# Kernel tuning notes

Hardware: AMD Instinct MI355X
Metric: run time of the kernel (lower is better)

Reference implementation:

```python
import jax, jax.numpy as jnp
import numpy as np

B, S, E, H = 4, 2048, 1024, 16
D = E // H  # head_dim = 64


def setup_inputs() -> dict:
    key = jax.random.key(0)
    ks = jax.random.split(key, 5)
    return {
        "hidden_states": jax.random.normal(ks[0], (B, S, E), dtype=jnp.float32),
        "c_attn_w": jax.random.normal(ks[1], (E, 3 * E), dtype=jnp.float32) * 0.02,
        "c_attn_b": jax.random.normal(ks[2], (3 * E,), dtype=jnp.float32) * 0.02,
        "c_proj_w": jax.random.normal(ks[3], (E, E), dtype=jnp.float32) * 0.02,
        "c_proj_b": jax.random.normal(ks[4], (E,), dtype=jnp.float32) * 0.02,
    }


def reference(hidden_states, c_attn_w, c_attn_b, c_proj_w, c_proj_b):
    b, s, e = hidden_states.shape
    # Conv1D c_attn: y = x @ W + b  -> qkv [b, s, 3E]
    qkv = hidden_states @ c_attn_w + c_attn_b
    q, k, v = jnp.split(qkv, 3, axis=-1)
    # split heads -> [b, H, s, D]
    def split_heads(t):
        return t.reshape(b, s, H, D).transpose(0, 2, 1, 3)
    q, k, v = split_heads(q), split_heads(k), split_heads(v)
    # QK^T scaled by sqrt(head_dim)
    scores = jnp.einsum("bhqd,bhkd->bhqk", q, k) / jnp.sqrt(
        jnp.asarray(D, dtype=q.dtype)
    )
    # causal mask (tril), masked positions get dtype min
    causal = jnp.tril(jnp.ones((s, s), dtype=bool))[None, None]
    mask_value = jnp.finfo(scores.dtype).min
    scores = jnp.where(causal, scores, mask_value)
    attn = jax.nn.softmax(scores, axis=-1)
    # attend to values, merge heads
    out = jnp.einsum("bhqk,bhkd->bhqd", attn, v)
    out = out.transpose(0, 2, 1, 3).reshape(b, s, e)
    # Conv1D c_proj
    return out @ c_proj_w + c_proj_b
```

## Files before the change

### kernel.cpp

```cpp
#include <hip/hip_runtime.h>
#include <hip/hip_bf16.h>
#include <cstdint>
#include <cstddef>

#define BB 4
#define SS 2048
#define EE 1024
#define HH 16
#define DD 64

typedef __attribute__((ext_vector_type(8))) short bf16x8;
typedef __attribute__((ext_vector_type(4))) float f32x4;

__device__ __forceinline__ short f2bf(float f) {
    union { float f; uint32_t u; } x; x.f = f;
    uint32_t r = (x.u + 0x7fffu + ((x.u >> 16) & 1u)) >> 16;
    return (short)r;
}
__device__ __forceinline__ short f2bf_fast(float f) {
    union { float f; uint32_t u; } x; x.f = f;
    return (short)((x.u + 0x8000u) >> 16);
}

__device__ __forceinline__ void gload16(const void* g, void* l) {
    __builtin_amdgcn_global_load_lds(
        (__attribute__((address_space(1))) uint32_t*)(uintptr_t)g,
        (__attribute__((address_space(3))) uint32_t*)(uint32_t)(uintptr_t)l,
        16, 0, 0);
}

#define WAIT_BARRIER(N)                                          \
    asm volatile("s_waitcnt vmcnt(" #N ")" ::: "memory");        \
    __builtin_amdgcn_s_barrier();                                \
    __builtin_amdgcn_sched_barrier(0);

template<int CTRL>
__device__ __forceinline__ float dppmove(float v) {
    return __int_as_float(__builtin_amdgcn_update_dpp(
        0, __float_as_int(v), CTRL, 0xf, 0xf, true));
}
#define ROW_REDUCE(vals, OP)                                             \
    _Pragma("unroll") for (int _r = 0; _r < 4; ++_r) {                   \
        vals[_r] = OP(vals[_r], dppmove<0xB1>(vals[_r]));                \
        vals[_r] = OP(vals[_r], dppmove<0x4E>(vals[_r]));                \
        vals[_r] = OP(vals[_r], dppmove<0x124>(vals[_r]));               \
        vals[_r] = OP(vals[_r], dppmove<0x128>(vals[_r]));               \
    }
__device__ __forceinline__ float opmax(float a, float b) { return fmaxf(a, b); }
__device__ __forceinline__ float opsum(float a, float b) { return a + b; }

__global__ void prep_kernel(const float* __restrict__ hs, short* __restrict__ Xb,
                            const float* __restrict__ attn_w, short* __restrict__ WqkvT,
                            const float* __restrict__ proj_w, short* __restrict__ WprojT)
{
    __shared__ float ts[32][33];
    int bid = blockIdx.x;
    const int t = threadIdx.x;
    if (bid < 2048) {
        const int n4 = (BB * SS * EE) / 4;
        const int stride = 2048 * 256;
        for (int i = bid * 256 + t; i < n4; i += stride) {
            float4 v = reinterpret_cast<const float4*>(hs)[i];
            short4 o;
            o.x = f2bf(v.x); o.y = f2bf(v.y); o.z = f2bf(v.z); o.w = f2bf(v.w);
            reinterpret_cast<short4*>(Xb)[i] = o;
        }
        return;
    }
    bid -= 2048;
    const float* in; short* out; int ncols, bx, by;
    if (bid < 3072) { in = attn_w; out = WqkvT; ncols = 3 * EE; bx = bid % 96; by = bid / 96; }
    else { bid -= 3072; in = proj_w; out = WprojT; ncols = EE; bx = bid % 32; by = bid / 32; }
    const int r = t >> 3, c4 = (t & 7) * 4;
    const int n0 = bx * 32, k0 = by * 32;
    float4 v = *reinterpret_cast<const float4*>(&in[(size_t)(k0 + r) * ncols + n0 + c4]);
    ts[c4 + 0][r] = v.x; ts[c4 + 1][r] = v.y; ts[c4 + 2][r] = v.z; ts[c4 + 3][r] = v.w;
    __syncthreads();
    short4 ov;
    ov.x = f2bf(ts[r][c4 + 0]); ov.y = f2bf(ts[r][c4 + 1]);
    ov.z = f2bf(ts[r][c4 + 2]); ov.w = f2bf(ts[r][c4 + 3]);
    *reinterpret_cast<short4*>(&out[(size_t)(n0 + r) * EE + k0 + c4]) = ov;
}

template<int MODE>
__global__ __launch_bounds__(256, 2)
void gemm128(const short* __restrict__ A, const short* __restrict__ Bt,
             const float* __restrict__ bias,
             short* __restrict__ Qo, short* __restrict__ Ko, short* __restrict__ Vo,
             float* __restrict__ Co)
{
    __shared__ short As[3][4096];
    __shared__ short Bs[3][4096];
    const int tid  = threadIdx.x;
    const int lane = tid & 63, wid = tid >> 6;
    const int wr = wid >> 1, wc = wid & 1;
    const int l15 = lane & 15, lhi = lane >> 4;
    const int m0 = blockIdx.y * 128, n0 = blockIdx.x * 128;
    const int sr   = lane >> 2;
    const int scol = 8 * ((lane & 3) ^ ((lane >> 3) & 3));
    const int rdx  = (lhi ^ ((l15 >> 1) & 3)) << 4;

    f32x4 acc[4][4] = {};

#define G_STAGE(tt, bufi)                                                        \
    {                                                                            \
        const int kk = (tt) * 32;                                                \
        _Pragma("unroll")                                                        \
        for (int p = 0; p < 2; ++p) {                                            \
            const int c = wid * 2 + p;                                           \
            gload16(&A [(size_t)(m0 + c * 16 + sr) * EE + kk + scol],            \
                    (char*)&As[bufi][0] + c * 1024);                             \
            gload16(&Bt[(size_t)(n0 + c * 16 + sr) * EE + kk + scol],            \
                    (char*)&Bs[bufi][0] + c * 1024);                             \
        }                                                                        \
    }

    G_STAGE(0, 0)
    G_STAGE(1, 1)
    WAIT_BARRIER(4)

    for (int kt = 0; kt < 32; ++kt) {
        const int cur = kt % 3;
        if (kt + 2 < 32) { const int nb = (kt + 2) % 3; G_STAGE(kt + 2, nb) }

        bf16x8 af[4], bfr[4];
        #pragma unroll
        for (int mm = 0; mm < 4; ++mm)
            af[mm] = *reinterpret_cast<const bf16x8*>(
                (const char*)&As[cur][0] + (wr * 64 + mm * 16 + l15) * 64 + rdx);
        #pragma unroll
        for (int nn = 0; nn < 4; ++nn)
            bfr[nn] = *reinterpret_cast<const bf16x8*>(
                (const char*)&Bs[cur][0] + (wc * 64 + nn * 16 + l15) * 64 + rdx);
        #pragma unroll
        for (int mm = 0; mm < 4; ++mm)
            #pragma unroll
            for (int nn = 0; nn < 4; ++nn)
                acc[mm][nn] = __builtin_amdgcn_mfma_f32_16x16x32_bf16(af[mm], bfr[nn], acc[mm][nn], 0, 0, 0);

        if (kt < 30)       { WAIT_BARRIER(4) }
        else if (kt == 30) { WAIT_BARRIER(0) }
    }
#undef G_STAGE

    if (MODE == 0) {
        const int part = n0 >> 10;
        #pragma unroll
        for (int mm = 0; mm < 4; ++mm) {
            #pragma unroll
            for (int nn = 0; nn < 4; ++nn) {
                const int gcol = n0 + wc * 64 + nn * 16 + l15;
                const float bv = bias[gcol];
                const int e = gcol & 1023;
                const int h = e >> 6, d = e & 63;
                const int grow0 = m0 + wr * 64 + mm * 16 + lhi * 4;
                const int bidx = grow0 >> 11;
                const int s0 = grow0 & 2047;
                const int bh = bidx * HH + h;
                if (part == 2) {
                    short4 pk;
                    pk.x = f2bf(acc[mm][nn][0] + bv);
                    pk.y = f2bf(acc[mm][nn][1] + bv);
                    pk.z = f2bf(acc[mm][nn][2] + bv);
                    pk.w = f2bf(acc[mm][nn][3] + bv);
                    *reinterpret_cast<short4*>(&Vo[((size_t)bh * DD + d) * SS + s0]) = pk;
                } else if (part == 0) {
                    #pragma unroll
                    for (int r = 0; r < 4; ++r)
                        Qo[((size_t)bh * SS + s0 + r) * DD + d] = f2bf((acc[mm][nn][r] + bv) * 0.18033688f);
                } else {
                    #pragma unroll
                    for (int r = 0; r < 4; ++r)
                        Ko[((size_t)bh * SS + s0 + r) * DD + d] = f2bf(acc[mm][nn][r] + bv);
                }
            }
        }
    } else {
        #pragma unroll
        for (int mm = 0; mm < 4; ++mm) {
            #pragma unroll
            for (int nn = 0; nn < 4; ++nn) {
                const int gcol = n0 + wc * 64 + nn * 16 + l15;
                const float bv = bias[gcol];
                #pragma unroll
                for (int r = 0; r < 4; ++r) {
                    const int grow = m0 + wr * 64 + mm * 16 + lhi * 4 + r;
                    Co[(size_t)grow * EE + gcol] = acc[mm][nn][r] + bv;
                }
            }
        }
    }
}

__global__ __launch_bounds__(512, 2)
void attn_kernel(const short* __restrict__ Q, const short* __restrict__ K,
                 const short* __restrict__ Vt, short* __restrict__ CTX)
{
    __shared__ short Ks[2][4096];
    __shared__ short Vs[2][4096];
    __shared__ short Ps[8][1024];
    const int tid  = threadIdx.x;
    const int lane = tid & 63, wid = tid >> 6;
    const int l15 = lane & 15, lhi = lane >> 4;
    const int bid  = blockIdx.x;
    const int bh   = (bid & 7) * 8 + ((bid >> 3) & 7);
    const int pair = bid >> 6;
    const int b = bh >> 4, h = bh & 15;
    const size_t base = (size_t)bh * (SS * DD);
    const short* VtBase = Vt + (size_t)bh * (DD * SS);
    char* const pw = (char*)&Ps[wid][0];

    const int srow = lane >> 3;
    const int scol = 8 * ((lane & 7) ^ srow);

    for (int phase = 0; phase < 2; ++phase) {
        const int t = phase ? (15 - pair) : pair;
        const int q0 = t * 128;
        const int qbase = q0 + wid * 16;
        const int nkt = 2 * t + 2;

        bf16x8 qa[2];
        qa[0] = *reinterpret_cast<const bf16x8*>(&Q[base + (size_t)(qbase + l15) * DD + lhi * 8]);
        qa[1] = *reinterpret_cast<const bf16x8*>(&Q[base + (size_t)(qbase + l15) * DD + 32 + lhi * 8]);

        f32x4 o[4] = {};
        float lrow[4] = {0.f, 0.f, 0.f, 0.f};

        gload16(&K     [base + (size_t)(wid * 8 + srow) * DD + scol], (char*)&Ks[0][0] + wid * 1024);
        gload16(&VtBase[(size_t)(wid * 8 + srow) * SS + scol],        (char*)&Vs[0][0] + wid * 1024);
        __syncthreads();

        for (int kt = 0; kt < nkt; ++kt) {
            const int cur = kt & 1;
            const int k0 = kt * 64;

            f32x4 sc[4];
            #pragma unroll
            for (int n = 0; n < 4; ++n) {
                const int row = n * 16 + l15;
                f32x4 cacc = {};
                #pragma unroll
                for (int ks = 0; ks < 2; ++ks) {
                    const int byteoff = (ks * 64 + lhi * 16) ^ ((l15 & 7) << 4);
                    bf16x8 kb = *reinterpret_cast<const bf16x8*>((const char*)&Ks[cur][0] + row * 128 + byteoff);
                    cacc = __builtin_amdgcn_mfma_f32_16x16x32_bf16(qa[ks], kb, cacc, 0, 0, 0);
                }
                sc[n] = cacc;
            }

            if (kt + 1 < nkt) {
                const int k1 = k0 + 64;
                gload16(&K     [base + (size_t)(k1 + wid * 8 + srow) * DD + scol],
                        (char*)&Ks[cur ^ 1][0] + wid * 1024);
                gload16(&VtBase[(size_t)(wid * 8 + srow) * SS + k1 + scol],
                        (char*)&Vs[cur ^ 1][0] + wid * 1024);
            }

            if (k0 + 63 > qbase) {
                #pragma unroll
                for (int n = 0; n < 4; ++n) {
                    const int col = k0 + n * 16 + l15;
                    #pragma unroll
                    for (int r = 0; r < 4; ++r) {
                        const int qrow = qbase + lhi * 4 + r;
                        if (col > qrow) sc[n][r] = -1e30f;
                    }
                }
            }
            #pragma unroll
            for (int n = 0; n < 4; ++n)
                #pragma unroll
                for (int r = 0; r < 4; ++r) sc[n][r] = __builtin_amdgcn_exp2f(sc[n][r]);
            #pragma unroll
            for (int n = 0; n < 4; ++n)
                #pragma unroll
                for (int r = 0; r < 4; ++r) {
                    const int q = lhi * 4 + r;
                    const int cb = (n * 32 + l15 * 2) ^ ((q & 7) << 4);
                    *reinterpret_cast<short*>(pw + q * 128 + cb) = f2bf_fast(sc[n][r]);
                }
            bf16x8 pa[2];
            #pragma unroll
            for (int ks = 0; ks < 2; ++ks)
                pa[ks] = *reinterpret_cast<const bf16x8*>(
                    pw + l15 * 128 + ((ks * 64 + lhi * 16) ^ ((l15 & 7) << 4)));
            #pragma unroll
            for (int dg = 0; dg < 4; ++dg) {
                const int row = dg * 16 + l15;
                #pragma unroll
                for (int ks = 0; ks < 2; ++ks) {
                    const int byteoff = (ks * 64 + lhi * 16) ^ ((l15 & 7) << 4);
                    bf16x8 vb = *reinterpret_cast<const bf16x8*>((const char*)&Vs[cur][0] + row * 128 + byteoff);
                    o[dg] = __builtin_amdgcn_mfma_f32_16x16x32_bf16(pa[ks], vb, o[dg], 0, 0, 0);
                }
            }
            float tsum[4];
            #pragma unroll
            for (int r = 0; r < 4; ++r)
                tsum[r] = (sc[0][r] + sc[1][r]) + (sc[2][r] + sc[3][r]);
            ROW_REDUCE(tsum, opsum)
            #pragma unroll
            for (int r = 0; r < 4; ++r) lrow[r] += tsum[r];

            __syncthreads();
        }

        #pragma unroll
        for (int dg = 0; dg < 4; ++dg)
            #pragma unroll
            for (int r = 0; r < 4; ++r) {
                int s = qbase + lhi * 4 + r;
                float val = o[dg][r] / lrow[r];
                CTX[(size_t)(b * SS + s) * EE + h * DD + dg * 16 + l15] = f2bf(val);
            }
    }
}

extern "C" void kernel_launch(void* const* d_in, const int* in_sizes, int n_in,
                              void* d_out, int out_size, void* d_ws, size_t ws_size,
                              hipStream_t stream) {
    const float* hs     = (const float*)d_in[0];
    const float* attn_w = (const float*)d_in[1];
    const float* attn_b = (const float*)d_in[2];
    const float* proj_w = (const float*)d_in[3];
    const float* proj_b = (const float*)d_in[4];
    float* out = (float*)d_out;

    char* ws = (char*)d_ws;
    short* Xb    = (short*)(ws + 0);
    short* WqkvT = (short*)(ws + 16777216);
    short* WprojT= (short*)(ws + 23068672);
    short* Qb    = (short*)(ws + 25165824);
    short* Kb    = (short*)(ws + 41943040);
    short* Vb    = (short*)(ws + 58720256);
    short* CTX   = Xb;

    prep_kernel<<<dim3(2048 + 3072 + 1024), dim3(256), 0, stream>>>(
        hs, Xb, attn_w, WqkvT, proj_w, WprojT);

    gemm128<0><<<dim3(3 * EE / 128, BB * SS / 128), dim3(256), 0, stream>>>(
        Xb, WqkvT, attn_b, Qb, Kb, Vb, nullptr);

    attn_kernel<<<dim3(512), dim3(512), 0, stream>>>(Qb, Kb, Vb, CTX);

    gemm128<1><<<dim3(EE / 128, BB * SS / 128), dim3(256), 0, stream>>>(
        CTX, WprojT, proj_b, nullptr, nullptr, nullptr, out);
}
```

Baseline: 169.3 us.

## Triple-buffer K/V tiles in attention and defer row-sum reduction to the end

The attention loop moves from double to triple buffering of the K and V^T LDS tiles. Each iteration prefetches two tiles ahead and uses a counted wait plus barrier (WAIT_BARRIER) instead of a full __syncthreads. The per-iteration cross-lane row-sum reduction is replaced by per-lane partial sums reduced once after the loop. This aims to hide global-load latency and cut per-tile shuffle work, at the cost of more LDS per block, which may reduce occupancy at 2 blocks per CU.

```diff
diff --git a/kernel.cpp b/kernel.cpp
--- a/kernel.cpp
+++ b/kernel.cpp
@@ -196,8 +196,8 @@
 void attn_kernel(const short* __restrict__ Q, const short* __restrict__ K,
                  const short* __restrict__ Vt, short* __restrict__ CTX)
 {
-    __shared__ short Ks[2][4096];
-    __shared__ short Vs[2][4096];
+    __shared__ short Ks[3][4096];
+    __shared__ short Vs[3][4096];
     __shared__ short Ps[8][1024];
     const int tid  = threadIdx.x;
     const int lane = tid & 63, wid = tid >> 6;
@@ -213,6 +213,15 @@
     const int srow = lane >> 3;
     const int scol = 8 * ((lane & 7) ^ srow);
 
+#define ATT_STAGE(tt, bufi)                                                          \
+    {                                                                                \
+        const int kk = (tt) * 64;                                                    \
+        gload16(&K[base + (size_t)(kk + wid * 8 + srow) * DD + scol],                \
+                (char*)&Ks[bufi][0] + wid * 1024);                                   \
+        gload16(&VtBase[(size_t)(wid * 8 + srow) * SS + kk + scol],                  \
+                (char*)&Vs[bufi][0] + wid * 1024);                                   \
+    }
+
     for (int phase = 0; phase < 2; ++phase) {
         const int t = phase ? (15 - pair) : pair;
         const int q0 = t * 128;
@@ -224,14 +233,14 @@
         qa[1] = *reinterpret_cast<const bf16x8*>(&Q[base + (size_t)(qbase + l15) * DD + 32 + lhi * 8]);
 
         f32x4 o[4] = {};
-        float lrow[4] = {0.f, 0.f, 0.f, 0.f};
-
-        gload16(&K     [base + (size_t)(wid * 8 + srow) * DD + scol], (char*)&Ks[0][0] + wid * 1024);
-        gload16(&VtBase[(size_t)(wid * 8 + srow) * SS + scol],        (char*)&Vs[0][0] + wid * 1024);
-        __syncthreads();
+        float psum[4] = {0.f, 0.f, 0.f, 0.f};
+
+        ATT_STAGE(0, 0)
+        ATT_STAGE(1, 1)
+        WAIT_BARRIER(2)
 
         for (int kt = 0; kt < nkt; ++kt) {
-            const int cur = kt & 1;
+            const int cur = kt % 3;
             const int k0 = kt * 64;
 
             f32x4 sc[4];
@@ -248,13 +257,7 @@
                 sc[n] = cacc;
             }
 
-            if (kt + 1 < nkt) {
-                const int k1 = k0 + 64;
-                gload16(&K     [base + (size_t)(k1 + wid * 8 + srow) * DD + scol],
-                        (char*)&Ks[cur ^ 1][0] + wid * 1024);
-                gload16(&VtBase[(size_t)(wid * 8 + srow) * SS + k1 + scol],
-                        (char*)&Vs[cur ^ 1][0] + wid * 1024);
-            }
+            if (kt + 2 < nkt) { ATT_STAGE(kt + 2, (kt + 2) % 3) }
 
             if (k0 + 63 > qbase) {
                 #pragma unroll
@@ -272,6 +275,9 @@
                 #pragma unroll
                 for (int r = 0; r < 4; ++r) sc[n][r] = __builtin_amdgcn_exp2f(sc[n][r]);
             #pragma unroll
+            for (int r = 0; r < 4; ++r)
+                psum[r] += (sc[0][r] + sc[1][r]) + (sc[2][r] + sc[3][r]);
+            #pragma unroll
             for (int n = 0; n < 4; ++n)
                 #pragma unroll
                 for (int r = 0; r < 4; ++r) {
@@ -294,16 +300,16 @@
                     o[dg] = __builtin_amdgcn_mfma_f32_16x16x32_bf16(pa[ks], vb, o[dg], 0, 0, 0);
                 }
             }
-            float tsum[4];
-            #pragma unroll
-            for (int r = 0; r < 4; ++r)
-                tsum[r] = (sc[0][r] + sc[1][r]) + (sc[2][r] + sc[3][r]);
-            ROW_REDUCE(tsum, opsum)
-            #pragma unroll
-            for (int r = 0; r < 4; ++r) lrow[r] += tsum[r];
-
-            __syncthreads();
+
+            if (kt < nkt - 2)       { WAIT_BARRIER(2) }
+            else if (kt == nkt - 2) { WAIT_BARRIER(0) }
         }
+        __syncthreads();
+
+        float lrow[4];
+        #pragma unroll
+        for (int r = 0; r < 4; ++r) lrow[r] = psum[r];
+        ROW_REDUCE(lrow, opsum)
 
         #pragma unroll
         for (int dg = 0; dg < 4; ++dg)
@@ -314,6 +320,7 @@
                 CTX[(size_t)(b * SS + s) * EE + h * DD + dg * 16 + l15] = f2bf(val);
             }
     }
+#undef ATT_STAGE
 }
 
 extern "C" void kernel_launch(void* const* d_in, const int* in_sizes, int n_in,
```

New measurement: 165.3 us. 1.02x faster.
